# Optimization experiments

Hardware: AMD Instinct MI355X
Metric: run time of the kernel (lower is better)

Reference implementation:

```python
import jax, jax.numpy as jnp
import numpy as np

SCALE = 1.0 / np.sqrt(512.0).astype(np.float32)  # attention() hardcodes d_k=512


def setup_inputs() -> dict:
    key = jax.random.key(0)
    ks = jax.random.split(key, 9)
    B, S, D = 4, 2048, 512
    mk = lambda k, shape: jax.random.normal(k, shape, dtype=jnp.float32) * 0.05
    return {
        "q": mk(ks[0], (B, S, D)),
        "k": mk(ks[1], (B, S, D)),
        "v": mk(ks[2], (B, S, D)),
        "WQ_w": mk(ks[3], (D, D)),
        "WQ_b": mk(ks[4], (D,)),
        "WK_w": mk(ks[5], (D, D)),
        "WK_b": mk(ks[6], (D,)),
        "WV_w": mk(ks[7], (D, D)),
        "WV_b": mk(ks[8], (D,)),
    }


def reference(q, k, v, WQ_w, WQ_b, WK_w, WK_b, WV_w, WV_b):
    # torch nn.Linear: y = x @ W.T + b
    qp = q @ WQ_w.T + WQ_b  # [B,S,dk]
    kp = k @ WK_w.T + WK_b  # [B,S,dk]
    vp = v @ WV_w.T + WV_b  # [B,S,dv]
    qk = jnp.einsum("bqd,bkd->bqk", qp, kp) * SCALE  # [B,Sq,Sk]
    S = qk.shape[1]
    tril = jnp.tril(jnp.ones((S, S), dtype=qk.dtype))  # multiplicative causal mask
    qk = qk * tril
    # NOTE: original applies softmax over dim=1 (the query axis), faithfully kept.
    attn = jax.nn.softmax(qk, axis=1)
    out = jnp.einsum("bqk,bkd->bqd", attn, vp)  # [B,Sq,dv]
    return out
```

## Files before the change

### kernel.cpp

```cpp
#include <hip/hip_runtime.h>
#include <hip/hip_bf16.h>


#define S_LEN 2048
#define D_DIM 512
#define SCALE_F 0.044194173824159216f

typedef __attribute__((ext_vector_type(8))) short s8v;
typedef __attribute__((ext_vector_type(4))) short s4v;
typedef __attribute__((ext_vector_type(4))) float f4v;

enum { EPI_BIAS = 0, EPI_BIAS_T = 1, EPI_SCORES = 2 };

#define SBAR()    asm volatile("s_barrier" ::: "memory")
#define WAITV(n)  asm volatile("s_waitcnt vmcnt(" #n ")" ::: "memory")

__device__ __forceinline__ short f2bf_s(float f) {
  union { __hip_bfloat16 b; short s; } u; u.b = __float2bfloat16(f); return u.s;
}
__device__ __forceinline__ float bf2f_s(short h) {
  union { short s; __hip_bfloat16 b; } u; u.s = h; return __bfloat162float(u.b);
}

__device__ __forceinline__ void glds16(const short* g, short* l) {
  __builtin_amdgcn_global_load_lds((const __attribute__((address_space(1))) void*)g,
                                   (__attribute__((address_space(3))) void*)l, 16, 0, 0);
}

template <int EPI>
__device__ __forceinline__ void gemm_core(
    const short* __restrict__ A, const short* __restrict__ B,
    short* __restrict__ C, const float* __restrict__ bias,
    short* SMEM, int N, int K, size_t sCz, int m0, int n0, int bz,
    float* __restrict__ Z)
{
  const int tid  = threadIdx.x;
  const int w    = tid >> 6;
  const int lane = tid & 63;
  const int quad = lane >> 4;
  const int l16  = lane & 15;
  const int wm   = (w >> 1) * 64;
  const int wn   = (w & 1) * 64;

  const int strow = tid >> 2;
  const int gl = ((tid & 3) ^ (strow & 3)) * 8;

  f4v acc[4][4];
#pragma unroll
  for (int i = 0; i < 4; ++i)
#pragma unroll
    for (int j = 0; j < 4; ++j)
#pragma unroll
      for (int r = 0; r < 4; ++r) acc[i][j][r] = 0.0f;

  const short* Ag = A + (size_t)(m0 + strow) * K + gl;
  const short* Bg = B + (size_t)(n0 + strow) * K + gl;
  const size_t pstr = (size_t)64 * K;
  const int t8 = tid * 8;
  const int swq = l16 & 3;

  const int niter = K >> 5;

#pragma unroll
  for (int p = 0; p < 2; ++p) glds16(Ag + p * pstr, SMEM + t8 + p * 2048);
#pragma unroll
  for (int p = 0; p < 2; ++p) glds16(Bg + p * pstr, SMEM + 4096 + t8 + p * 2048);

  for (int i = 0; i < niter; ++i) {
    const int c = i & 1;
    if (i + 1 < niter) {
      const int k1 = (i + 1) << 5;
      short* dA = SMEM + (1 - c) * 8192 + t8;
#pragma unroll
      for (int p = 0; p < 2; ++p) glds16(Ag + k1 + p * pstr, dA + p * 2048);
#pragma unroll
      for (int p = 0; p < 2; ++p) glds16(Bg + k1 + p * pstr, dA + 4096 + p * 2048);
      WAITV(4);
    } else {
      WAITV(0);
    }
    SBAR();

    const short* As = SMEM + c * 8192;
    const short* Bs = As + 4096;
    s8v af[4], bf[4];
#pragma unroll
    for (int ii = 0; ii < 4; ++ii)
      af[ii] = *(const s8v*)&As[(wm + ii * 16 + l16) * 32 + ((quad ^ swq) * 8)];
#pragma unroll
    for (int j = 0; j < 4; ++j)
      bf[j] = *(const s8v*)&Bs[(wn + j * 16 + l16) * 32 + ((quad ^ swq) * 8)];
#pragma unroll
    for (int ii = 0; ii < 4; ++ii)
#pragma unroll
      for (int j = 0; j < 4; ++j)
        acc[ii][j] = __builtin_amdgcn_mfma_f32_16x16x32_bf16(af[ii], bf[j], acc[ii][j], 0, 0, 0);
    SBAR();
  }

  float bv[4];
  if (EPI == EPI_BIAS || EPI == EPI_BIAS_T) {
#pragma unroll
    for (int j = 0; j < 4; ++j) bv[j] = bias[n0 + wn + j * 16 + l16];
  }

  if (EPI == EPI_BIAS_T) {
#pragma unroll
    for (int i = 0; i < 4; ++i) {
#pragma unroll
      for (int j = 0; j < 4; ++j) {
        const int gn  = n0 + wn + j * 16 + l16;
        const int gmb = m0 + wm + i * 16 + quad * 4;
        const int bb = gmb >> 11, ssb = gmb & (S_LEN - 1);
        s4v o;
#pragma unroll
        for (int r = 0; r < 4; ++r) o[r] = f2bf_s(acc[i][j][r] + bv[j]);
        *(s4v*)&C[((size_t)bb * D_DIM + gn) * S_LEN + ssb] = o;
      }
    }
    return;
  }

  short* TB = SMEM;
  const int wbase = w * 2176;
  float csum[4] = {0.f, 0.f, 0.f, 0.f};

#pragma unroll
  for (int ph = 0; ph < 2; ++ph) {
    __syncthreads();
#pragma unroll
    for (int ii = 0; ii < 2; ++ii) {
      const int i = ph * 2 + ii;
#pragma unroll
      for (int j = 0; j < 4; ++j) {
        const int gn = n0 + wn + j * 16 + l16;
#pragma unroll
        for (int r = 0; r < 4; ++r) {
          short o;
          if (EPI == EPI_SCORES) {
            const int gm = m0 + wm + i * 16 + quad * 4 + r;
            const float f = (gm >= gn) ? (__expf(acc[i][j][r] * SCALE_F) - 1.0f) : 0.0f;
            csum[j] += f;
            o = f2bf_s(f);
          } else {
            o = f2bf_s(acc[i][j][r] + bv[j]);
          }
          TB[wbase + (ii * 16 + quad * 4 + r) * 68 + j * 16 + l16] = o;
        }
      }
    }
    __syncthreads();
#pragma unroll
    for (int p = 0; p < 4; ++p) {
      const int row = p * 8 + (lane >> 3);
      const int cg  = lane & 7;
      const s8v vv = *(const s8v*)&TB[wbase + row * 68 + cg * 8];
      const int gm = m0 + wm + ph * 32 + row;
      const int gn = n0 + wn + cg * 8;
      *(s8v*)&C[sCz + (size_t)gm * N + gn] = vv;
    }
  }

  if (EPI == EPI_SCORES) {
#pragma unroll
    for (int j = 0; j < 4; ++j) {
      float cs = csum[j];
      cs += __shfl_xor(cs, 16, 64);
      cs += __shfl_xor(cs, 32, 64);
      if (quad == 0) atomicAdd(&Z[(bz << 11) + n0 + wn + j * 16 + l16], cs);
    }
  }
}

__global__ __launch_bounds__(256, 4) void gemm_scoresF(
    const short* __restrict__ A, const short* __restrict__ B, short* __restrict__ C,
    float* __restrict__ Z)
{
  __shared__ __align__(16) short SMEM[16384];
  const int bz = blockIdx.z;
  const int t = blockIdx.x;
  int ti = (int)((sqrtf(8.0f * t + 1.0f) - 1.0f) * 0.5f);
  while ((ti + 1) * (ti + 2) / 2 <= t) ++ti;
  while (ti * (ti + 1) / 2 > t) --ti;
  const int tj = t - ti * (ti + 1) / 2;
  gemm_core<EPI_SCORES>(A + (size_t)bz * S_LEN * D_DIM, B + (size_t)bz * S_LEN * D_DIM,
                        C, nullptr, SMEM, S_LEN, D_DIM,
                        (size_t)bz * S_LEN * S_LEN, ti * 128, tj * 128, bz, Z);
}

__global__ __launch_bounds__(256, 4) void proj3(
    const short* __restrict__ a0, const short* __restrict__ a1, const short* __restrict__ a2,
    const short* __restrict__ b0, const short* __restrict__ b1, const short* __restrict__ b2,
    short* __restrict__ c0, short* __restrict__ c1, short* __restrict__ c2,
    const float* __restrict__ x0, const float* __restrict__ x1, const float* __restrict__ x2)
{
  __shared__ __align__(16) short SMEM[16384];
  const int z = blockIdx.z;
  const short* A = (z == 0) ? a0 : (z == 1) ? a1 : a2;
  const short* B = (z == 0) ? b0 : (z == 1) ? b1 : b2;
  short*       C = (z == 0) ? c0 : (z == 1) ? c1 : c2;
  const float* bias = (z == 0) ? x0 : (z == 1) ? x1 : x2;
  if (z == 2)
    gemm_core<EPI_BIAS_T>(A, B, C, bias, SMEM, D_DIM, D_DIM, 0,
                          blockIdx.y * 128, blockIdx.x * 128, 0, nullptr);
  else
    gemm_core<EPI_BIAS>(A, B, C, bias, SMEM, D_DIM, D_DIM, 0,
                        blockIdx.y * 128, blockIdx.x * 128, 0, nullptr);
}

__global__ __launch_bounds__(256, 2) void gemm_outF(
    const short* __restrict__ F, const short* __restrict__ vpT,
    const float* __restrict__ Tv, float* __restrict__ out)
{
  __shared__ __align__(16) short SMEM[36864];

  const int tid  = threadIdx.x;
  const int bz   = blockIdx.y;
  const int zs   = blockIdx.z;
  const int mi   = (zs < 16) ? (31 - zs) : (zs - 16);
  const int m0   = mi * 64;
  const int n0   = blockIdx.x * 128;

  const short* A = F   + (size_t)bz * S_LEN * S_LEN;
  const short* B = vpT + (size_t)bz * D_DIM * S_LEN;

  const int w    = tid >> 6;
  const int lane = tid & 63;
  const int quad = lane >> 4;
  const int l16  = lane & 15;
  const int wm   = (w >> 1) * 32;
  const int wn   = (w & 1) * 64;

  const int strow = tid >> 3;
  const int gl = ((tid & 7) ^ (strow & 7)) * 8;

  f4v acc[2][4];
#pragma unroll
  for (int i = 0; i < 2; ++i)
#pragma unroll
    for (int j = 0; j < 4; ++j)
#pragma unroll
      for (int r = 0; r < 4; ++r) acc[i][j][r] = 0.0f;

  const short* Ag = A + (size_t)(m0 + strow) * S_LEN + gl;
  const short* Bg = B + (size_t)(n0 + strow) * S_LEN + gl;
  const size_t pstr = (size_t)32 * S_LEN;
  const int t8 = tid * 8;
  const int swq = l16 & 7;

  const int niter = (m0 >> 6) + 1;

#pragma unroll
  for (int pre = 0; pre < 2; ++pre) {
    short* dst = SMEM + pre * 12288 + t8;
    const int k0 = pre << 6;
#pragma unroll
    for (int p = 0; p < 2; ++p) glds16(Ag + k0 + p * pstr, dst + p * 2048);
#pragma unroll
    for (int p = 0; p < 4; ++p) glds16(Bg + k0 + p * pstr, dst + 4096 + p * 2048);
  }

  int cbuf = 0, nbuf = 2;
  for (int i = 0; i < niter; ++i) {
    if (i + 2 < niter) {
      const int k2 = (i + 2) << 6;
      short* dst = SMEM + nbuf * 12288 + t8;
#pragma unroll
      for (int p = 0; p < 2; ++p) glds16(Ag + k2 + p * pstr, dst + p * 2048);
#pragma unroll
      for (int p = 0; p < 4; ++p) glds16(Bg + k2 + p * pstr, dst + 4096 + p * 2048);
      nbuf = (nbuf == 2) ? 0 : nbuf + 1;
      WAITV(12);
    } else if (i + 1 < niter) {
      WAITV(6);
    } else {
      WAITV(0);
    }
    SBAR();

    const short* As = SMEM + cbuf * 12288;
    const short* Bs = As + 4096;
    cbuf = (cbuf == 2) ? 0 : cbuf + 1;
#pragma unroll
    for (int kk = 0; kk < 2; ++kk) {
      s8v af[2], bf[4];
#pragma unroll
      for (int ii = 0; ii < 2; ++ii)
        af[ii] = *(const s8v*)&As[(wm + ii * 16 + l16) * 64 + (((kk * 4 + quad) ^ swq) * 8)];
#pragma unroll
      for (int j = 0; j < 4; ++j)
        bf[j] = *(const s8v*)&Bs[(wn + j * 16 + l16) * 64 + (((kk * 4 + quad) ^ swq) * 8)];
#pragma unroll
      for (int ii = 0; ii < 2; ++ii)
#pragma unroll
        for (int j = 0; j < 4; ++j)
          acc[ii][j] = __builtin_amdgcn_mfma_f32_16x16x32_bf16(af[ii], bf[j], acc[ii][j], 0, 0, 0);
    }
    SBAR();
  }

  float* Cf = out + (size_t)bz * S_LEN * D_DIM;
#pragma unroll
  for (int i = 0; i < 2; ++i) {
#pragma unroll
    for (int j = 0; j < 4; ++j) {
      const int gn = n0 + wn + j * 16 + l16;
      const float tvn = Tv[(bz << 9) + gn];
#pragma unroll
      for (int r = 0; r < 4; ++r) {
        const int gm = m0 + wm + i * 16 + quad * 4 + r;
        Cf[(size_t)gm * D_DIM + gn] = acc[i][j][r] + tvn;
      }
    }
  }
}

__global__ __launch_bounds__(256) void cvt3(
    const float* __restrict__ s0, const float* __restrict__ s1,
    const float* __restrict__ s2, short* __restrict__ dst, int n)
{
  const float* s = (blockIdx.y == 0) ? s0 : (blockIdx.y == 1) ? s1 : s2;
  short* d = dst + (size_t)blockIdx.y * n;
  const int i = (blockIdx.x * 256 + threadIdx.x) * 8;
  if (i >= n) return;
  const float4 f0 = *(const float4*)(s + i);
  const float4 f1 = *(const float4*)(s + i + 4);
  s8v o;
  o[0] = f2bf_s(f0.x); o[1] = f2bf_s(f0.y); o[2] = f2bf_s(f0.z); o[3] = f2bf_s(f0.w);
  o[4] = f2bf_s(f1.x); o[5] = f2bf_s(f1.y); o[6] = f2bf_s(f1.z); o[7] = f2bf_s(f1.w);
  *(s8v*)(d + i) = o;
}

__global__ __launch_bounds__(256) void scale_vpt_T(
    short* __restrict__ vpT, const float* __restrict__ ZF, float* __restrict__ Tv)
{
  __shared__ float red[4];
  const int b = blockIdx.y, d = blockIdx.x, tid = threadIdx.x;
  const size_t rowbase = ((size_t)(b * D_DIM + d)) * S_LEN;
  const float* zf = ZF + (b << 11);
  const int k0 = tid * 8;

  s8v v = *(s8v*)&vpT[rowbase + k0];
  float s = 0.0f;
#pragma unroll
  for (int i = 0; i < 8; ++i) {
    const float w = bf2f_s(v[i]) / (2048.0f + zf[k0 + i]);
    s += w;
    v[i] = f2bf_s(w);
  }
  *(s8v*)&vpT[rowbase + k0] = v;

#pragma unroll
  for (int off = 32; off >= 1; off >>= 1) s += __shfl_xor(s, off, 64);
  if ((tid & 63) == 0) red[tid >> 6] = s;
  __syncthreads();
  if (tid == 0) Tv[(b << 9) + d] = red[0] + red[1] + red[2] + red[3];
}

extern "C" void kernel_launch(void* const* d_in, const int* in_sizes, int n_in,
                              void* d_out, int out_size, void* d_ws, size_t ws_size,
                              hipStream_t stream) {
  const float* q   = (const float*)d_in[0];
  const float* k   = (const float*)d_in[1];
  const float* v   = (const float*)d_in[2];
  const float* WQw = (const float*)d_in[3];
  const float* WQb = (const float*)d_in[4];
  const float* WKw = (const float*)d_in[5];
  const float* WKb = (const float*)d_in[6];
  const float* WVw = (const float*)d_in[7];
  const float* WVb = (const float*)d_in[8];

  char* ws = (char*)d_ws;
  short* F   = (short*)(ws);
  short* qb  = (short*)(ws);
  short* Wqb = (short*)(ws + 25165824);
  short* qp  = (short*)(ws + 33554432);
  short* kp  = (short*)(ws + 41943040);
  short* vpT = (short*)(ws + 50331648);
  float* ZF  = (float*)(ws + 58720256);
  float* Tv  = (float*)(ws + 58753024);
  short* kb  = qb + 4194304;
  short* vb  = qb + 8388608;
  short* Wkb = Wqb + 262144;
  short* Wvb = Wqb + 524288;

  const dim3 blk(256);

  hipMemsetAsync(ZF, 0, 4 * S_LEN * sizeof(float), stream);

  cvt3<<<dim3(2048, 3), blk, 0, stream>>>(q, k, v, qb, 4194304);
  cvt3<<<dim3(128, 3), blk, 0, stream>>>(WQw, WKw, WVw, Wqb, 262144);

  proj3<<<dim3(4, 64, 3), blk, 0, stream>>>(
      qb, kb, vb, Wqb, Wkb, Wvb, qp, kp, vpT, WQb, WKb, WVb);

  gemm_scoresF<<<dim3(136, 1, 4), blk, 0, stream>>>(qp, kp, F, ZF);

  scale_vpt_T<<<dim3(512, 4), blk, 0, stream>>>(vpT, ZF, Tv);

  gemm_outF<<<dim3(4, 4, 32), blk, 0, stream>>>(F, vpT, Tv, (float*)d_out);
}
```

Measured before the change: 175.5 us.

## Triple-buffer GEMM core and drop trailing barrier per k-iteration

```diff
diff --git a/kernel.cpp b/kernel.cpp
--- a/kernel.cpp
+++ b/kernel.cpp
@@ -62,27 +62,34 @@
   const int niter = K >> 5;
 
 #pragma unroll
-  for (int p = 0; p < 2; ++p) glds16(Ag + p * pstr, SMEM + t8 + p * 2048);
-#pragma unroll
-  for (int p = 0; p < 2; ++p) glds16(Bg + p * pstr, SMEM + 4096 + t8 + p * 2048);
-
+  for (int t = 0; t < 2; ++t) {
+    const int k0 = t << 5;
+    short* dst = SMEM + t * 8192 + t8;
+#pragma unroll
+    for (int p = 0; p < 2; ++p) glds16(Ag + k0 + p * pstr, dst + p * 2048);
+#pragma unroll
+    for (int p = 0; p < 2; ++p) glds16(Bg + k0 + p * pstr, dst + 4096 + p * 2048);
+  }
+
+  int cb = 0;
   for (int i = 0; i < niter; ++i) {
-    const int c = i & 1;
-    if (i + 1 < niter) {
-      const int k1 = (i + 1) << 5;
-      short* dA = SMEM + (1 - c) * 8192 + t8;
-#pragma unroll
-      for (int p = 0; p < 2; ++p) glds16(Ag + k1 + p * pstr, dA + p * 2048);
-#pragma unroll
-      for (int p = 0; p < 2; ++p) glds16(Bg + k1 + p * pstr, dA + 4096 + p * 2048);
-      WAITV(4);
-    } else {
-      WAITV(0);
-    }
+    if (i + 1 < niter) { WAITV(4); } else { WAITV(0); }
     SBAR();
 
-    const short* As = SMEM + c * 8192;
+    if (i + 2 < niter) {
+      int nb = cb + 2; if (nb >= 3) nb -= 3;
+      const int k2 = (i + 2) << 5;
+      short* dst = SMEM + nb * 8192 + t8;
+#pragma unroll
+      for (int p = 0; p < 2; ++p) glds16(Ag + k2 + p * pstr, dst + p * 2048);
+#pragma unroll
+      for (int p = 0; p < 2; ++p) glds16(Bg + k2 + p * pstr, dst + 4096 + p * 2048);
+    }
+
+    const short* As = SMEM + cb * 8192;
     const short* Bs = As + 4096;
+    cb = (cb == 2) ? 0 : cb + 1;
+
     s8v af[4], bf[4];
 #pragma unroll
     for (int ii = 0; ii < 4; ++ii)
@@ -95,7 +102,6 @@
 #pragma unroll
       for (int j = 0; j < 4; ++j)
         acc[ii][j] = __builtin_amdgcn_mfma_f32_16x16x32_bf16(af[ii], bf[j], acc[ii][j], 0, 0, 0);
-    SBAR();
   }
 
   float bv[4];
@@ -172,11 +178,11 @@
   }
 }
 
-__global__ __launch_bounds__(256, 4) void gemm_scoresF(
+__global__ __launch_bounds__(256, 3) void gemm_scoresF(
     const short* __restrict__ A, const short* __restrict__ B, short* __restrict__ C,
     float* __restrict__ Z)
 {
-  __shared__ __align__(16) short SMEM[16384];
+  __shared__ __align__(16) short SMEM[24576];
   const int bz = blockIdx.z;
   const int t = blockIdx.x;
   int ti = (int)((sqrtf(8.0f * t + 1.0f) - 1.0f) * 0.5f);
@@ -188,13 +194,13 @@
                         (size_t)bz * S_LEN * S_LEN, ti * 128, tj * 128, bz, Z);
 }
 
-__global__ __launch_bounds__(256, 4) void proj3(
+__global__ __launch_bounds__(256, 3) void proj3(
     const short* __restrict__ a0, const short* __restrict__ a1, const short* __restrict__ a2,
     const short* __restrict__ b0, const short* __restrict__ b1, const short* __restrict__ b2,
     short* __restrict__ c0, short* __restrict__ c1, short* __restrict__ c2,
     const float* __restrict__ x0, const float* __restrict__ x1, const float* __restrict__ x2)
 {
-  __shared__ __align__(16) short SMEM[16384];
+  __shared__ __align__(16) short SMEM[24576];
   const int z = blockIdx.z;
   const short* A = (z == 0) ? a0 : (z == 1) ? a1 : a2;
   const short* B = (z == 0) ? b0 : (z == 1) ? b1 : b2;
@@ -260,23 +266,20 @@
     for (int p = 0; p < 4; ++p) glds16(Bg + k0 + p * pstr, dst + 4096 + p * 2048);
   }
 
-  int cbuf = 0, nbuf = 2;
+  int cbuf = 0;
   for (int i = 0; i < niter; ++i) {
+    if (i + 1 < niter) { WAITV(6); } else { WAITV(0); }
+    SBAR();
+
     if (i + 2 < niter) {
+      int nb = cbuf + 2; if (nb >= 3) nb -= 3;
       const int k2 = (i + 2) << 6;
-      short* dst = SMEM + nbuf * 12288 + t8;
+      short* dst = SMEM + nb * 12288 + t8;
 #pragma unroll
       for (int p = 0; p < 2; ++p) glds16(Ag + k2 + p * pstr, dst + p * 2048);
 #pragma unroll
       for (int p = 0; p < 4; ++p) glds16(Bg + k2 + p * pstr, dst + 4096 + p * 2048);
-      nbuf = (nbuf == 2) ? 0 : nbuf + 1;
-      WAITV(12);
-    } else if (i + 1 < niter) {
-      WAITV(6);
-    } else {
-      WAITV(0);
-    }
-    SBAR();
+    }
 
     const short* As = SMEM + cbuf * 12288;
     const short* Bs = As + 4096;
@@ -296,7 +299,6 @@
         for (int j = 0; j < 4; ++j)
           acc[ii][j] = __builtin_amdgcn_mfma_f32_16x16x32_bf16(af[ii], bf[j], acc[ii][j], 0, 0, 0);
     }
-    SBAR();
   }
 
   float* Cf = out + (size_t)bz * S_LEN * D_DIM;
```

Result: no change. 176.1 us (+0.4%).
